# Performance work log

Hardware: AMD Instinct MI355X
Metric: run time of the kernel (lower is better)

The kernel has to match this reference:

```python
import jax, jax.numpy as jnp
import numpy as np

DIM_IN, DIM_Q, DIM_K = 1024, 128, 128
B, S = 8, 2048

def setup_inputs() -> dict:
    key = jax.random.key(0)
    ks = jax.random.split(key, 9)
    sq = 1.0 / np.sqrt(DIM_IN)
    return {
        "query": jax.random.normal(ks[0], (B, S, DIM_IN), jnp.float32),
        "key": jax.random.normal(ks[1], (B, S, DIM_IN), jnp.float32),
        "value": jax.random.normal(ks[2], (B, S, DIM_IN), jnp.float32),
        "Wq": jax.random.uniform(ks[3], (DIM_IN, DIM_Q), jnp.float32, -sq, sq),
        "bq": jax.random.uniform(ks[4], (DIM_Q,), jnp.float32, -sq, sq),
        "Wk": jax.random.uniform(ks[5], (DIM_IN, DIM_K), jnp.float32, -sq, sq),
        "bk": jax.random.uniform(ks[6], (DIM_K,), jnp.float32, -sq, sq),
        "Wv": jax.random.uniform(ks[7], (DIM_IN, DIM_K), jnp.float32, -sq, sq),
        "bv": jax.random.uniform(ks[8], (DIM_K,), jnp.float32, -sq, sq),
    }

def reference(query, key, value, Wq, bq, Wk, bk, Wv, bv):
    q = jnp.einsum("bsd,dq->bsq", query, Wq) + bq          # [B,S,Dq]
    k = jnp.einsum("bsd,dk->bsk", key, Wk) + bk            # [B,S,Dk]
    v = jnp.einsum("bsd,dk->bsk", value, Wv) + bv          # [B,S,Dk]
    scale = jnp.asarray(q.shape[-1] ** 0.5, q.dtype)
    scores = jnp.einsum("bqd,bkd->bqk", q, k) / scale      # [B,S,S]
    attn = jax.nn.softmax(scores, axis=-1)
    return jnp.einsum("bqk,bkd->bqd", attn, v)             # [B,S,Dk]
```

## Files before the change

### kernel.cpp

```cpp
#include <hip/hip_runtime.h>

typedef __attribute__((ext_vector_type(8))) short short8;
typedef __attribute__((ext_vector_type(4))) float floatx4;

#define MFMA16(a, b, c) __builtin_amdgcn_mfma_f32_16x16x32_bf16(a, b, c, 0, 0, 0)

__device__ __forceinline__ short f2bf(float f) {
    unsigned int u = __float_as_uint(f);
    u = u + 0x7fffu + ((u >> 16) & 1u);
    return (short)(u >> 16);
}

__device__ __forceinline__ void ldst16(const void* g, void* l) {
    __builtin_amdgcn_global_load_lds(
        (const __attribute__((address_space(1))) void*)g,
        (__attribute__((address_space(3))) void*)l, 16, 0, 0);
}

__global__ __launch_bounds__(256) void wconv_kernel(const float* __restrict__ Wq,
                                                    const float* __restrict__ Wk,
                                                    const float* __restrict__ Wv,
                                                    short* __restrict__ wt) {
    int idx = blockIdx.x * 256 + threadIdx.x;
    int w = idx >> 17;
    int rem = idx & 131071;
    int k = rem >> 7, n = rem & 127;
    const float* W = (w == 0) ? Wq : (w == 1) ? Wk : Wv;
    wt[w * 131072 + n * 1024 + k] = f2bf(W[rem]);
}

__global__ __launch_bounds__(128) void proj_kernel(const float* __restrict__ Q,
                                                   const float* __restrict__ K,
                                                   const float* __restrict__ V,
                                                   const short* __restrict__ wt,
                                                   const float* __restrict__ bq,
                                                   const float* __restrict__ bk,
                                                   const float* __restrict__ bv,
                                                   short* __restrict__ qo,
                                                   short* __restrict__ ko,
                                                   short* __restrict__ vo) {
    const int t = threadIdx.x;
    const int wv = t >> 6, L = t & 63;
    const int q4 = L >> 4, l16 = L & 15;
    const int which = blockIdx.y;
    const float* A = (which == 0) ? Q : (which == 1) ? K : V;
    const short* Wt = wt + which * 131072;
    const float* bias = (which == 0) ? bq : (which == 1) ? bk : bv;
    const int m0 = blockIdx.x * 64 + wv * 32;

    floatx4 acc[2][8];
#pragma unroll
    for (int rg = 0; rg < 2; rg++)
#pragma unroll
        for (int nt = 0; nt < 8; nt++) acc[rg][nt] = (floatx4)0.0f;

    const float* a0 = A + (size_t)(m0 + l16) * 1024 + 8 * q4;
    const float* a1 = a0 + 16 * 1024;
    const short* wb = Wt + (size_t)l16 * 1024 + 8 * q4;

    float4 pa[2][2][2];
#pragma unroll
    for (int rg = 0; rg < 2; rg++) {
        const float* ap = rg ? a1 : a0;
#pragma unroll
        for (int ks = 0; ks < 2; ks++) {
            pa[rg][ks][0] = *(const float4*)(ap + 32 * ks);
            pa[rg][ks][1] = *(const float4*)(ap + 32 * ks + 4);
        }
    }

    for (int k0 = 0; k0 < 1024; k0 += 64) {
        short8 af[2][2];
#pragma unroll
        for (int rg = 0; rg < 2; rg++)
#pragma unroll
            for (int ks = 0; ks < 2; ks++) {
                float4 f0 = pa[rg][ks][0], f1 = pa[rg][ks][1];
                short8 v;
                v[0] = f2bf(f0.x); v[1] = f2bf(f0.y); v[2] = f2bf(f0.z); v[3] = f2bf(f0.w);
                v[4] = f2bf(f1.x); v[5] = f2bf(f1.y); v[6] = f2bf(f1.z); v[7] = f2bf(f1.w);
                af[rg][ks] = v;
            }
        if (k0 + 64 < 1024) {
#pragma unroll
            for (int rg = 0; rg < 2; rg++) {
                const float* ap = (rg ? a1 : a0) + k0 + 64;
#pragma unroll
                for (int ks = 0; ks < 2; ks++) {
                    pa[rg][ks][0] = *(const float4*)(ap + 32 * ks);
                    pa[rg][ks][1] = *(const float4*)(ap + 32 * ks + 4);
                }
            }
        }
#pragma unroll
        for (int ks = 0; ks < 2; ks++)
#pragma unroll
            for (int nt = 0; nt < 8; nt++) {
                short8 bf = *(const short8*)(wb + (size_t)nt * 16384 + k0 + 32 * ks);
                acc[0][nt] = MFMA16(af[0][ks], bf, acc[0][nt]);
                acc[1][nt] = MFMA16(af[1][ks], bf, acc[1][nt]);
            }
    }

#pragma unroll
    for (int rg = 0; rg < 2; rg++) {
        const int rbase = m0 + rg * 16 + q4 * 4;
#pragma unroll
        for (int nt = 0; nt < 8; nt++) {
            const int col = 16 * nt + l16;
            float bvv = bias[col];
#pragma unroll
            for (int r = 0; r < 4; r++) {
                short h = f2bf(acc[rg][nt][r] + bvv);
                int grow = rbase + r;
                if (which == 0) {
                    qo[(size_t)grow * 128 + col] = h;
                } else if (which == 1) {
                    ko[(size_t)grow * 128 + col] = h;
                } else {
                    int bb = grow >> 11, s = grow & 2047;
                    vo[(size_t)bb * 262144 + (size_t)col * 2048 + s] = h;
                }
            }
        }
    }
}

__global__ __launch_bounds__(512, 2) void flash_kernel(const short* __restrict__ qw,
                                                       const short* __restrict__ kw,
                                                       const short* __restrict__ vw,
                                                       float* __restrict__ out) {
    alignas(16) __shared__ short Kls[2][64 * 128];
    alignas(16) __shared__ short Vls[2][128 * 64];
    alignas(16) __shared__ short Pl[2][64][72];
    const int t = threadIdx.x;
    const int wvi = t >> 6, L = t & 63;
    const int pr = wvi >> 2, wq = wvi & 3;
    const int pt = t & 255;
    const int q4 = L >> 4, l16 = L & 15;
    const int bq = blockIdx.x, b = blockIdx.y;
    const short* qp = qw + (size_t)b * 262144 + (size_t)bq * 64 * 128;
    const short* kp = kw + (size_t)b * 262144;
    const short* vp = vw + (size_t)b * 262144;

    short8 qf[4];
    for (int ks = 0; ks < 4; ks++)
        qf[ks] = *(const short8*)(qp + (16 * wq + l16) * 128 + ks * 32 + q4 * 8);

    floatx4 oacc[8];
    for (int dt = 0; dt < 8; dt++) oacc[dt] = (floatx4)0.0f;
    float ps[4] = {0.f, 0.f, 0.f, 0.f};
    const float SL = (float)(0.08838834764831845 * 1.4426950408889634);

    for (int kt = 0; kt < 16; kt++) {
        const int kv0 = pr * 1024 + kt * 64;
        __syncthreads();
        for (int j = 0; j < 4; j++) {
            int s = j * 256 + pt;
            int r = s >> 4, c = (s & 15) ^ (r & 15);
            ldst16(kp + (size_t)(kv0 + r) * 128 + c * 8,
                   &Kls[pr][(j * 256 + 64 * wq) * 8]);
        }
        for (int j = 0; j < 4; j++) {
            int s = j * 256 + pt;
            int r = s >> 3, c = (s & 7) ^ (r & 7);
            ldst16(vp + (size_t)r * 2048 + kv0 + c * 8,
                   &Vls[pr][(j * 256 + 64 * wq) * 8]);
        }
        __syncthreads();

        floatx4 sa[4];
        for (int nt = 0; nt < 4; nt++) {
            sa[nt] = (floatx4)0.0f;
            for (int ks = 0; ks < 4; ks++) {
                short8 bfr = *(short8*)&Kls[pr][(16 * nt + l16) * 128 + ((4 * ks + q4) ^ l16) * 8];
                sa[nt] = MFMA16(qf[ks], bfr, sa[nt]);
            }
        }

        for (int nt = 0; nt < 4; nt++) {
            for (int r = 0; r < 4; r++) {
                float pv = __builtin_amdgcn_exp2f(sa[nt][r] * SL - 4.0f);
                ps[r] += pv;
                Pl[pr][16 * wq + q4 * 4 + r][16 * nt + l16] = f2bf(pv);
            }
        }

        short8 pf0 = *(short8*)&Pl[pr][16 * wq + l16][q4 * 8];
        short8 pf1 = *(short8*)&Pl[pr][16 * wq + l16][32 + q4 * 8];
        for (int dt = 0; dt < 8; dt++) {
            short8 v0 = *(short8*)&Vls[pr][(16 * dt + l16) * 64 + (q4 ^ (l16 & 7)) * 8];
            short8 v1 = *(short8*)&Vls[pr][(16 * dt + l16) * 64 + ((4 + q4) ^ (l16 & 7)) * 8];
            oacc[dt] = MFMA16(pf0, v0, oacc[dt]);
            oacc[dt] = MFMA16(pf1, v1, oacc[dt]);
        }
    }

    for (int r = 0; r < 4; r++)
        for (int off = 1; off <= 8; off <<= 1)
            ps[r] += __shfl_xor(ps[r], off, 64);

    __syncthreads();
    float* Om = (float*)&Kls[0][0];
    float* Lm = (float*)&Vls[0][0];
    if (pr == 1) {
        for (int dt = 0; dt < 8; dt++)
            for (int r = 0; r < 4; r++)
                Om[(16 * wq + q4 * 4 + r) * 128 + 16 * dt + l16] = oacc[dt][r];
        if (l16 == 0)
            for (int r = 0; r < 4; r++)
                Lm[16 * wq + q4 * 4 + r] = ps[r];
    }
    __syncthreads();
    if (pr == 0) {
        float inv[4];
        for (int r = 0; r < 4; r++)
            inv[r] = 1.0f / (ps[r] + Lm[16 * wq + q4 * 4 + r]);
        for (int dt = 0; dt < 8; dt++) {
            for (int r = 0; r < 4; r++) {
                int row = 16 * wq + q4 * 4 + r;
                int qrow = bq * 64 + row;
                out[((size_t)b * 2048 + qrow) * 128 + 16 * dt + l16] =
                    (oacc[dt][r] + Om[row * 128 + 16 * dt + l16]) * inv[r];
            }
        }
    }
}

extern "C" void kernel_launch(void* const* d_in, const int* in_sizes, int n_in,
                              void* d_out, int out_size, void* d_ws, size_t ws_size,
                              hipStream_t stream) {
    const float* query = (const float*)d_in[0];
    const float* key   = (const float*)d_in[1];
    const float* value = (const float*)d_in[2];
    const float* Wq    = (const float*)d_in[3];
    const float* bq    = (const float*)d_in[4];
    const float* Wk    = (const float*)d_in[5];
    const float* bk    = (const float*)d_in[6];
    const float* Wv    = (const float*)d_in[7];
    const float* bv    = (const float*)d_in[8];
    float* out = (float*)d_out;

    short* wt  = (short*)d_ws;
    short* qws = wt + 3 * 131072;
    short* kws = qws + 16384 * 128;
    short* vws = kws + 16384 * 128;

    wconv_kernel<<<1536, 256, 0, stream>>>(Wq, Wk, Wv, wt);
    proj_kernel<<<dim3(256, 3), 128, 0, stream>>>(query, key, value, wt,
                                                  bq, bk, bv, qws, kws, vws);
    flash_kernel<<<dim3(32, 8), 512, 0, stream>>>(qws, kws, vws, out);
}
```

Measured before the change: 282.0 us.

## Stage projection input through double-buffered LDS and restructure flash kernel tiling

The projection kernel now uses 256 threads with a 2x2 wave split and stages the fp32 input tile into a double-buffered, XOR-swizzled LDS buffer via global_load_lds. The flash kernel shrinks to 32 query rows per block with 256 threads and double-buffers K tiles in LDS so the next tile's load overlaps compute, removing one barrier per step. V is no longer staged and is read straight from global memory for the PV MFMA. Many loops are explicitly unrolled. This raises the grid size and overlap, but V reads become uncoalesced global loads and K is now re-read by twice as many blocks.

Result: slower. 325.4 us (+15.4%).

```diff
diff --git a/kernel.cpp b/kernel.cpp
--- a/kernel.cpp
+++ b/kernel.cpp
@@ -29,73 +29,69 @@
     wt[w * 131072 + n * 1024 + k] = f2bf(W[rem]);
 }
 
-__global__ __launch_bounds__(128) void proj_kernel(const float* __restrict__ Q,
-                                                   const float* __restrict__ K,
-                                                   const float* __restrict__ V,
-                                                   const short* __restrict__ wt,
-                                                   const float* __restrict__ bq,
-                                                   const float* __restrict__ bk,
-                                                   const float* __restrict__ bv,
-                                                   short* __restrict__ qo,
-                                                   short* __restrict__ ko,
-                                                   short* __restrict__ vo) {
+__global__ __launch_bounds__(256, 2) void proj_kernel(const float* __restrict__ Q,
+                                                      const float* __restrict__ K,
+                                                      const float* __restrict__ V,
+                                                      const short* __restrict__ wt,
+                                                      const float* __restrict__ bq,
+                                                      const float* __restrict__ bk,
+                                                      const float* __restrict__ bv,
+                                                      short* __restrict__ qo,
+                                                      short* __restrict__ ko,
+                                                      short* __restrict__ vo) {
+    alignas(16) __shared__ float Asl[2][64 * 64];
     const int t = threadIdx.x;
     const int wv = t >> 6, L = t & 63;
+    const int wr = wv >> 1, wc = wv & 1;
     const int q4 = L >> 4, l16 = L & 15;
     const int which = blockIdx.y;
     const float* A = (which == 0) ? Q : (which == 1) ? K : V;
     const short* Wt = wt + which * 131072;
     const float* bias = (which == 0) ? bq : (which == 1) ? bk : bv;
-    const int m0 = blockIdx.x * 64 + wv * 32;
-
-    floatx4 acc[2][8];
+    const int m0 = blockIdx.x * 64;
+
+    floatx4 acc[2][4];
 #pragma unroll
     for (int rg = 0; rg < 2; rg++)
 #pragma unroll
-        for (int nt = 0; nt < 8; nt++) acc[rg][nt] = (floatx4)0.0f;
-
-    const float* a0 = A + (size_t)(m0 + l16) * 1024 + 8 * q4;
-    const float* a1 = a0 + 16 * 1024;
-    const short* wb = Wt + (size_t)l16 * 1024 + 8 * q4;
-
-    float4 pa[2][2][2];
-#pragma unroll
-    for (int rg = 0; rg < 2; rg++) {
-        const float* ap = rg ? a1 : a0;
-#pragma unroll
-        for (int ks = 0; ks < 2; ks++) {
-            pa[rg][ks][0] = *(const float4*)(ap + 32 * ks);
-            pa[rg][ks][1] = *(const float4*)(ap + 32 * ks + 4);
-        }
-    }
-
-    for (int k0 = 0; k0 < 1024; k0 += 64) {
+        for (int nt = 0; nt < 4; nt++) acc[rg][nt] = (floatx4)0.0f;
+
+    const short* wb = Wt + (size_t)(64 * wc + l16) * 1024 + 8 * q4;
+
+    auto stage = [&](int buf, int k0) {
+        for (int j = 0; j < 4; j++) {
+            int s = j * 256 + t;
+            int r = s >> 4, c = (s & 15) ^ (r & 15);
+            ldst16(A + (size_t)(m0 + r) * 1024 + k0 + c * 4,
+                   &Asl[buf][(j * 256 + 64 * wv) * 4]);
+        }
+    };
+
+    stage(0, 0);
+
+    for (int kc = 0; kc < 16; kc++) {
+        const int cur = kc & 1, k0 = kc * 64;
+        __syncthreads();
+        if (kc + 1 < 16) stage(cur ^ 1, k0 + 64);
+
         short8 af[2][2];
 #pragma unroll
         for (int rg = 0; rg < 2; rg++)
 #pragma unroll
             for (int ks = 0; ks < 2; ks++) {
-                float4 f0 = pa[rg][ks][0], f1 = pa[rg][ks][1];
+                int rl = 32 * wr + 16 * rg + l16;
+                int c0 = 8 * ks + 2 * q4;
+                float4 f0 = *(float4*)&Asl[cur][(rl * 16 + (c0 ^ l16)) * 4];
+                float4 f1 = *(float4*)&Asl[cur][(rl * 16 + ((c0 + 1) ^ l16)) * 4];
                 short8 v;
                 v[0] = f2bf(f0.x); v[1] = f2bf(f0.y); v[2] = f2bf(f0.z); v[3] = f2bf(f0.w);
                 v[4] = f2bf(f1.x); v[5] = f2bf(f1.y); v[6] = f2bf(f1.z); v[7] = f2bf(f1.w);
                 af[rg][ks] = v;
             }
-        if (k0 + 64 < 1024) {
-#pragma unroll
-            for (int rg = 0; rg < 2; rg++) {
-                const float* ap = (rg ? a1 : a0) + k0 + 64;
-#pragma unroll
-                for (int ks = 0; ks < 2; ks++) {
-                    pa[rg][ks][0] = *(const float4*)(ap + 32 * ks);
-                    pa[rg][ks][1] = *(const float4*)(ap + 32 * ks + 4);
-                }
-            }
-        }
 #pragma unroll
         for (int ks = 0; ks < 2; ks++)
 #pragma unroll
-            for (int nt = 0; nt < 8; nt++) {
+            for (int nt = 0; nt < 4; nt++) {
                 short8 bf = *(const short8*)(wb + (size_t)nt * 16384 + k0 + 32 * ks);
                 acc[0][nt] = MFMA16(af[0][ks], bf, acc[0][nt]);
                 acc[1][nt] = MFMA16(af[1][ks], bf, acc[1][nt]);
@@ -104,10 +100,10 @@
 
 #pragma unroll
     for (int rg = 0; rg < 2; rg++) {
-        const int rbase = m0 + rg * 16 + q4 * 4;
-#pragma unroll
-        for (int nt = 0; nt < 8; nt++) {
-            const int col = 16 * nt + l16;
+        const int rbase = m0 + 32 * wr + 16 * rg + q4 * 4;
+#pragma unroll
+        for (int nt = 0; nt < 4; nt++) {
+            const int col = 64 * wc + 16 * nt + l16;
             float bvv = bias[col];
 #pragma unroll
             for (int r = 0; r < 4; r++) {
@@ -126,59 +122,65 @@
     }
 }
 
-__global__ __launch_bounds__(512, 2) void flash_kernel(const short* __restrict__ qw,
+__global__ __launch_bounds__(256, 2) void flash_kernel(const short* __restrict__ qw,
                                                        const short* __restrict__ kw,
                                                        const short* __restrict__ vw,
                                                        float* __restrict__ out) {
-    alignas(16) __shared__ short Kls[2][64 * 128];
-    alignas(16) __shared__ short Vls[2][128 * 64];
-    alignas(16) __shared__ short Pl[2][64][72];
+    alignas(16) __shared__ short Kls[2][2][64 * 128];
+    alignas(16) __shared__ short Pl[2][32][72];
     const int t = threadIdx.x;
     const int wvi = t >> 6, L = t & 63;
-    const int pr = wvi >> 2, wq = wvi & 3;
-    const int pt = t & 255;
+    const int pr = wvi >> 1, wq = wvi & 1;
+    const int pt = t & 127;
     const int q4 = L >> 4, l16 = L & 15;
     const int bq = blockIdx.x, b = blockIdx.y;
-    const short* qp = qw + (size_t)b * 262144 + (size_t)bq * 64 * 128;
+    const short* qp = qw + (size_t)b * 262144 + (size_t)bq * 32 * 128;
     const short* kp = kw + (size_t)b * 262144;
     const short* vp = vw + (size_t)b * 262144;
 
     short8 qf[4];
+#pragma unroll
     for (int ks = 0; ks < 4; ks++)
         qf[ks] = *(const short8*)(qp + (16 * wq + l16) * 128 + ks * 32 + q4 * 8);
 
     floatx4 oacc[8];
+#pragma unroll
     for (int dt = 0; dt < 8; dt++) oacc[dt] = (floatx4)0.0f;
     float ps[4] = {0.f, 0.f, 0.f, 0.f};
     const float SL = (float)(0.08838834764831845 * 1.4426950408889634);
 
+    auto stage = [&](int buf, int kt) {
+        const int kv0 = pr * 1024 + kt * 64;
+        for (int j = 0; j < 8; j++) {
+            int s = j * 128 + pt;
+            int r = s >> 4, c = (s & 15) ^ (r & 15);
+            ldst16(kp + (size_t)(kv0 + r) * 128 + c * 8,
+                   &Kls[buf][pr][(j * 128 + 64 * wq) * 8]);
+        }
+    };
+
+    stage(0, 0);
+
     for (int kt = 0; kt < 16; kt++) {
+        const int cur = kt & 1;
         const int kv0 = pr * 1024 + kt * 64;
         __syncthreads();
-        for (int j = 0; j < 4; j++) {
-            int s = j * 256 + pt;
-            int r = s >> 4, c = (s & 15) ^ (r & 15);
-            ldst16(kp + (size_t)(kv0 + r) * 128 + c * 8,
-                   &Kls[pr][(j * 256 + 64 * wq) * 8]);
-        }
-        for (int j = 0; j < 4; j++) {
-            int s = j * 256 + pt;
-            int r = s >> 3, c = (s & 7) ^ (r & 7);
-            ldst16(vp + (size_t)r * 2048 + kv0 + c * 8,
-                   &Vls[pr][(j * 256 + 64 * wq) * 8]);
-        }
-        __syncthreads();
+        if (kt + 1 < 16) stage(cur ^ 1, kt + 1);
 
         floatx4 sa[4];
+#pragma unroll
         for (int nt = 0; nt < 4; nt++) {
             sa[nt] = (floatx4)0.0f;
+#pragma unroll
             for (int ks = 0; ks < 4; ks++) {
-                short8 bfr = *(short8*)&Kls[pr][(16 * nt + l16) * 128 + ((4 * ks + q4) ^ l16) * 8];
+                short8 bfr = *(short8*)&Kls[cur][pr][(16 * nt + l16) * 128 + ((4 * ks + q4) ^ l16) * 8];
                 sa[nt] = MFMA16(qf[ks], bfr, sa[nt]);
             }
         }
 
+#pragma unroll
         for (int nt = 0; nt < 4; nt++) {
+#pragma unroll
             for (int r = 0; r < 4; r++) {
                 float pv = __builtin_amdgcn_exp2f(sa[nt][r] * SL - 4.0f);
                 ps[r] += pv;
@@ -188,38 +190,47 @@
 
         short8 pf0 = *(short8*)&Pl[pr][16 * wq + l16][q4 * 8];
         short8 pf1 = *(short8*)&Pl[pr][16 * wq + l16][32 + q4 * 8];
+#pragma unroll
         for (int dt = 0; dt < 8; dt++) {
-            short8 v0 = *(short8*)&Vls[pr][(16 * dt + l16) * 64 + (q4 ^ (l16 & 7)) * 8];
-            short8 v1 = *(short8*)&Vls[pr][(16 * dt + l16) * 64 + ((4 + q4) ^ (l16 & 7)) * 8];
+            short8 v0 = *(const short8*)(vp + (size_t)(16 * dt + l16) * 2048 + kv0 + 8 * q4);
+            short8 v1 = *(const short8*)(vp + (size_t)(16 * dt + l16) * 2048 + kv0 + 32 + 8 * q4);
             oacc[dt] = MFMA16(pf0, v0, oacc[dt]);
             oacc[dt] = MFMA16(pf1, v1, oacc[dt]);
         }
     }
 
+#pragma unroll
     for (int r = 0; r < 4; r++)
+#pragma unroll
         for (int off = 1; off <= 8; off <<= 1)
             ps[r] += __shfl_xor(ps[r], off, 64);
 
     __syncthreads();
-    float* Om = (float*)&Kls[0][0];
-    float* Lm = (float*)&Vls[0][0];
+    float* Om = (float*)&Kls[0][0][0];
+    float* Lm = (float*)&Kls[1][0][0];
     if (pr == 1) {
+#pragma unroll
         for (int dt = 0; dt < 8; dt++)
+#pragma unroll
             for (int r = 0; r < 4; r++)
                 Om[(16 * wq + q4 * 4 + r) * 128 + 16 * dt + l16] = oacc[dt][r];
         if (l16 == 0)
+#pragma unroll
             for (int r = 0; r < 4; r++)
                 Lm[16 * wq + q4 * 4 + r] = ps[r];
     }
     __syncthreads();
     if (pr == 0) {
         float inv[4];
+#pragma unroll
         for (int r = 0; r < 4; r++)
             inv[r] = 1.0f / (ps[r] + Lm[16 * wq + q4 * 4 + r]);
+#pragma unroll
         for (int dt = 0; dt < 8; dt++) {
+#pragma unroll
             for (int r = 0; r < 4; r++) {
                 int row = 16 * wq + q4 * 4 + r;
-                int qrow = bq * 64 + row;
+                int qrow = bq * 32 + row;
                 out[((size_t)b * 2048 + qrow) * 128 + 16 * dt + l16] =
                     (oacc[dt][r] + Om[row * 128 + 16 * dt + l16]) * inv[r];
             }
@@ -247,7 +258,7 @@
     short* vws = kws + 16384 * 128;
 
     wconv_kernel<<<1536, 256, 0, stream>>>(Wq, Wk, Wv, wt);
-    proj_kernel<<<dim3(256, 3), 128, 0, stream>>>(query, key, value, wt,
+    proj_kernel<<<dim3(256, 3), 256, 0, stream>>>(query, key, value, wt,
                                                   bq, bk, bv, qws, kws, vws);
-    flash_kernel<<<dim3(32, 8), 512, 0, stream>>>(qws, kws, vws, out);
-}
+    flash_kernel<<<dim3(64, 8), 256, 0, stream>>>(qws, kws, vws, out);
+}
```
